# Kernel tuning notes

Hardware: AMD Instinct MI355X
Metric: run time of the kernel (lower is better)

## Reference

```python
import jax, jax.numpy as jnp
import numpy as np

N = 50000      # nodes
E = 800000     # edges (avg degree 16)
NFEAT = 256
NHID = 128
NCLASS = 40
NLAYERS_MID = 13  # gc2..gc14


def setup_inputs() -> dict:
    key = jax.random.key(0)
    ks = jax.random.split(key, 16)
    stdv_h = 1.0 / np.sqrt(NHID)     # GraphConvolution stdv = 1/sqrt(out_features)
    stdv_c = 1.0 / np.sqrt(NCLASS)
    u = lambda k, shape, s: jax.random.uniform(k, shape, jnp.float32, -s, s)
    return {
        "x": jax.random.normal(ks[0], (N, NFEAT), jnp.float32),
        "edge_src": jax.random.randint(ks[1], (E,), 0, N, jnp.int32),
        "edge_dst": jax.random.randint(ks[2], (E,), 0, N, jnp.int32),
        "edge_weight": jax.random.uniform(ks[3], (E,), jnp.float32),
        # skip-branch linear (self.weight / self.bias)
        "W0": u(ks[4], (NFEAT, NHID), stdv_h),
        "b0": u(ks[5], (NHID,), stdv_h),
        # gc1: nfeat -> nhid
        "W1": u(ks[6], (NFEAT, NHID), stdv_h),
        "b1": u(ks[7], (NHID,), stdv_h),
        # gc2..gc14: nhid -> nhid, stacked
        "Wmid": u(ks[8], (NLAYERS_MID, NHID, NHID), stdv_h),
        "bmid": u(ks[9], (NLAYERS_MID, NHID), stdv_h),
        # gc15: 14*nhid -> nclass
        "W15": u(ks[10], (14 * NHID, NCLASS), stdv_c),
        "b15": u(ks[11], (NCLASS,), stdv_c),
    }


def reference(x, edge_src, edge_dst, edge_weight, W0, b0, W1, b1, Wmid, bmid, W15, b15):
    n = x.shape[0]

    def gcn(h, W, b):
        # support = h @ W ; out = spmm(adj, support) + b  (adj as weighted edge list)
        support = h @ W
        msgs = support[edge_src] * edge_weight[:, None]           # [E, d]
        agg = jax.ops.segment_sum(msgs, edge_dst, num_segments=n)  # [N, d]
        return agg + b

    z = x @ W0 + b0
    x1 = jax.nn.relu(gcn(x, W1, b1)) + z

    def step(h, Wb):
        W, b = Wb
        hn = jax.nn.relu(gcn(h, W, b)) + h
        return hn, hn

    _, xs = jax.lax.scan(step, x1, (Wmid, bmid))   # xs: [13, N, NHID] = x2..x14
    all_x = jnp.concatenate([x1[None], xs], axis=0)  # [14, N, NHID] = x1..x14
    # concat order in torch code: (x14, x13, ..., x1)
    x_cat = jnp.swapaxes(all_x[::-1], 0, 1).reshape(n, 14 * NHID)
    # dropout is identity in eval mode
    x15 = gcn(x_cat, W15, b15)
    return jax.nn.log_softmax(x15, axis=1)
```

## Files before the change

kernel.cpp:

```cpp
#include <hip/hip_runtime.h>
#include <stdint.h>

#define NN 50000
#define EE 800000
#define DH 128
#define NC 40
#define KCAT (14*DH)
#define CAP 64

typedef __bf16 bf16x8 __attribute__((ext_vector_type(8)));
typedef float floatx4 __attribute__((ext_vector_type(4)));

#define GLOAD_LDS16(gp, lp)                                                          \
  __builtin_amdgcn_global_load_lds(                                                  \
      (const __attribute__((address_space(1))) uint32_t*)(gp),                       \
      (__attribute__((address_space(3))) uint32_t*)(lp), 16, 0, 0)

__device__ __forceinline__ float bf2f(unsigned short u) {
  union { uint32_t i; float f; } v; v.i = ((uint32_t)u) << 16; return v.f;
}
__device__ __forceinline__ unsigned short f2bf(float f) {
  union { float f; uint32_t i; } v; v.f = f;
  uint32_t x = v.i;
  uint32_t r = (x + 0x7fffu + ((x >> 16) & 1u)) >> 16;
  return (unsigned short)r;
}

__global__ void init_counts_detect(int* counts, const unsigned short* xw) {
  int i = blockIdx.x * blockDim.x + threadIdx.x;
  if (i < NN) counts[i] = 0;
  if (blockIdx.x == 0) {
    int t = threadIdx.x;
    int wild = 0;
    for (int k = t; k < 4096; k += 256) {
      unsigned e = (xw[k] >> 7) & 0xFF;
      if (e >= 0x90) wild++;
    }
    __shared__ int red[256];
    red[t] = wild;
    __syncthreads();
    for (int s = 128; s > 0; s >>= 1) {
      if (t < s) red[t] += red[t + s];
      __syncthreads();
    }
    if (t == 0) counts[NN] = red[0];
  }
}

__global__ void convert_f4(const void* in, unsigned short* outp, int n4, const int* flag) {
  bool isf32 = (*flag) > 32;
  for (int i = blockIdx.x * blockDim.x + threadIdx.x; i < n4;
       i += gridDim.x * blockDim.x) {
    ushort4 o;
    if (isf32) {
      float4 v = ((const float4*)in)[i];
      o.x = f2bf(v.x); o.y = f2bf(v.y); o.z = f2bf(v.z); o.w = f2bf(v.w);
    } else {
      o = ((const ushort4*)in)[i];
    }
    ((ushort4*)outp)[i] = o;
  }
}

__global__ void convert_bias(const void* b0, const void* b1, const void* bm,
                             const void* b15, unsigned short* bb, const int* flag) {
  bool isf32 = (*flag) > 32;
  int i = blockIdx.x * blockDim.x + threadIdx.x;
  if (i >= 1960) return;
  const void* src; int off;
  if (i < 128)        { src = b0;  off = i; }
  else if (i < 256)   { src = b1;  off = i - 128; }
  else if (i < 1920)  { src = bm;  off = i - 256; }
  else                { src = b15; off = i - 1920; }
  bb[i] = isf32 ? f2bf(((const float*)src)[off]) : ((const unsigned short*)src)[off];
}

__global__ void transpose_w(const void* B, unsigned short* BT,
                            int L, int K, int M, int Mpad, const int* flag) {
  bool isf32 = (*flag) > 32;
  int total = L * Mpad * K;
  for (int idx = blockIdx.x * blockDim.x + threadIdx.x; idx < total;
       idx += gridDim.x * blockDim.x) {
    int k = idx % K;
    int n = (idx / K) % Mpad;
    int l = idx / (K * Mpad);
    unsigned short v = 0;
    if (n < M) {
      size_t si = (size_t)l * K * M + (size_t)k * M + n;
      v = isf32 ? f2bf(((const float*)B)[si]) : ((const unsigned short*)B)[si];
    }
    BT[idx] = v;
  }
}

__global__ void build_ell(const int* __restrict__ src, const int* __restrict__ dst,
                          const void* __restrict__ w,
                          int* __restrict__ cnt, int2* __restrict__ ell,
                          const int* __restrict__ flag) {
  bool isf32 = (*flag) > 32;
  int e = blockIdx.x * blockDim.x + threadIdx.x;
  if (e >= EE) return;
  int d = dst[e];
  if ((unsigned)d >= NN) return;
  int p = atomicAdd(&cnt[d], 1);
  if (p >= CAP) return;
  int s = src[e];
  float wf = isf32 ? ((const float*)w)[e] : bf2f(((const unsigned short*)w)[e]);
  if ((unsigned)s >= NN) { s = 0; wf = 0.f; }
  union { float f; int i; } wv; wv.f = wf;
  ell[(size_t)d * CAP + p] = make_int2(s, wv.i);
}

__global__ __launch_bounds__(256) void gemm_first(
    const unsigned short* __restrict__ A,
    const unsigned short* __restrict__ BT,
    unsigned short* __restrict__ C0,
    unsigned short* __restrict__ C1,
    const unsigned short* __restrict__ bias) {
  __shared__ unsigned short As[64 * 256];
  int t = threadIdx.x;
  int wave = t >> 6, lane = t & 63;
  int q = lane >> 4, mn = lane & 15;
  int r0 = blockIdx.x * 64;

  #pragma unroll
  for (int cc = 0; cc < 8; ++cc) {
    int L = cc * 4096 + t * 16;
    int row = L >> 9;
    int colb = (L & 511) ^ ((row & 7) << 4);
    int gr = r0 + row; if (gr >= NN) gr = NN - 1;
    GLOAD_LDS16((const char*)A + (size_t)gr * 512 + colb, (char*)As + L);
  }
  __syncthreads();

  floatx4 acc[4][4];
  floatx4 zf = {0.f, 0.f, 0.f, 0.f};
  #pragma unroll
  for (int i = 0; i < 4; ++i)
    #pragma unroll
    for (int j = 0; j < 4; ++j) acc[i][j] = zf;

  #pragma unroll
  for (int ks = 0; ks < 8; ++ks) {
    bf16x8 fa[4], fb[4];
    #pragma unroll
    for (int i = 0; i < 4; ++i) {
      int row = i * 16 + mn;
      fa[i] = *(const bf16x8*)((const char*)As + row * 512 +
                               ((ks * 64 + q * 16) ^ ((row & 7) << 4)));
    }
    #pragma unroll
    for (int j = 0; j < 4; ++j)
      fb[j] = *(const bf16x8*)((const char*)BT +
                               (size_t)(wave * 64 + j * 16 + mn) * 512 + ks * 64 + q * 16);
    #pragma unroll
    for (int i = 0; i < 4; ++i)
      #pragma unroll
      for (int j = 0; j < 4; ++j)
        acc[i][j] = __builtin_amdgcn_mfma_f32_16x16x32_bf16(fa[i], fb[j], acc[i][j], 0, 0, 0);
  }

  #pragma unroll
  for (int j = 0; j < 4; ++j) {
    int col = wave * 64 + j * 16 + mn;
    bool is0 = col < 128;
    int ccol = is0 ? col : col - 128;
    unsigned short* Cp = is0 ? C0 : C1;
    float badd = is0 ? bf2f(bias[ccol]) : 0.f;
    #pragma unroll
    for (int i = 0; i < 4; ++i) {
      int rbase = r0 + i * 16 + q * 4;
      #pragma unroll
      for (int rr = 0; rr < 4; ++rr) {
        int row = rbase + rr;
        if (row < NN) Cp[(size_t)row * 128 + ccol] = f2bf(acc[i][j][rr] + badd);
      }
    }
  }
}

__global__ __launch_bounds__(256) void gemm_mid(
    const unsigned short* __restrict__ A,
    const unsigned short* __restrict__ BT,
    unsigned short* __restrict__ C) {
  __shared__ unsigned short As[32 * 128];
  int t = threadIdx.x;
  int wave = t >> 6, lane = t & 63;
  int q = lane >> 4, mn = lane & 15;
  int r0 = blockIdx.x * 32;

  #pragma unroll
  for (int cc = 0; cc < 2; ++cc) {
    int L = cc * 4096 + t * 16;
    int row = L >> 8;
    int colb = (L & 255) ^ ((row & 7) << 4);
    int gr = r0 + row; if (gr >= NN) gr = NN - 1;
    GLOAD_LDS16((const char*)A + (size_t)gr * (KCAT * 2) + colb, (char*)As + L);
  }
  __syncthreads();

  floatx4 acc[2][2];
  floatx4 zf = {0.f, 0.f, 0.f, 0.f};
  #pragma unroll
  for (int i = 0; i < 2; ++i)
    #pragma unroll
    for (int j = 0; j < 2; ++j) acc[i][j] = zf;

  #pragma unroll
  for (int ks = 0; ks < 4; ++ks) {
    bf16x8 fa[2], fb[2];
    #pragma unroll
    for (int i = 0; i < 2; ++i) {
      int row = i * 16 + mn;
      fa[i] = *(const bf16x8*)((const char*)As + row * 256 +
                               ((ks * 64 + q * 16) ^ ((row & 7) << 4)));
    }
    #pragma unroll
    for (int j = 0; j < 2; ++j)
      fb[j] = *(const bf16x8*)((const char*)BT +
                               (size_t)(wave * 32 + j * 16 + mn) * 256 + ks * 64 + q * 16);
    #pragma unroll
    for (int i = 0; i < 2; ++i)
      #pragma unroll
      for (int j = 0; j < 2; ++j)
        acc[i][j] = __builtin_amdgcn_mfma_f32_16x16x32_bf16(fa[i], fb[j], acc[i][j], 0, 0, 0);
  }

  #pragma unroll
  for (int i = 0; i < 2; ++i) {
    int rbase = r0 + i * 16 + q * 4;
    #pragma unroll
    for (int j = 0; j < 2; ++j) {
      int col = wave * 32 + j * 16 + mn;
      #pragma unroll
      for (int rr = 0; rr < 4; ++rr) {
        int row = rbase + rr;
        if (row < NN) C[(size_t)row * 128 + col] = f2bf(acc[i][j][rr]);
      }
    }
  }
}

__global__ __launch_bounds__(256) void gemm_cat2(
    const unsigned short* __restrict__ A,
    const unsigned short* __restrict__ BT,
    float* __restrict__ C) {
  __shared__ unsigned short As[2][64 * 128];
  int t = threadIdx.x;
  int wave = t >> 6, lane = t & 63;
  int q = lane >> 4, mn = lane & 15;
  int r0 = blockIdx.x * 64;

  floatx4 acc[3];
  floatx4 zf = {0.f, 0.f, 0.f, 0.f};
  #pragma unroll
  for (int j = 0; j < 3; ++j) acc[j] = zf;

  auto stage = [&](int c) {
    #pragma unroll
    for (int cc = 0; cc < 4; ++cc) {
      int L = cc * 4096 + t * 16;
      int row = L >> 8;
      int colb = (L & 255) ^ ((row & 7) << 4);
      int gr = r0 + row; if (gr >= NN) gr = NN - 1;
      GLOAD_LDS16((const char*)A + (size_t)gr * 3584 + c * 256 + colb,
                  (char*)As[c & 1] + L);
    }
  };

  stage(0);
  __syncthreads();
  for (int c = 0; c < 14; ++c) {
    if (c + 1 < 14) stage(c + 1);
    const char* buf = (const char*)As[c & 1];
    int rloc = wave * 16 + mn;
    int rsw = (rloc & 7) << 4;
    #pragma unroll
    for (int ks = 0; ks < 4; ++ks) {
      bf16x8 fa = *(const bf16x8*)(buf + rloc * 256 + ((ks * 64 + q * 16) ^ rsw));
      bf16x8 fb[3];
      #pragma unroll
      for (int j = 0; j < 3; ++j)
        fb[j] = *(const bf16x8*)((const char*)BT + (size_t)(j * 16 + mn) * 3584 +
                                 c * 256 + ks * 64 + q * 16);
      #pragma unroll
      for (int j = 0; j < 3; ++j)
        acc[j] = __builtin_amdgcn_mfma_f32_16x16x32_bf16(fa, fb[j], acc[j], 0, 0, 0);
    }
    if (c + 1 < 14) __syncthreads();
  }

  #pragma unroll
  for (int j = 0; j < 3; ++j) {
    int col = j * 16 + mn;
    if (col < NC) {
      #pragma unroll
      for (int rr = 0; rr < 4; ++rr) {
        int row = r0 + wave * 16 + q * 4 + rr;
        if (row < NN) C[(size_t)row * NC + col] = acc[j][rr];
      }
    }
  }
}

__global__ __launch_bounds__(256) void spmm_layer(
    const unsigned short* __restrict__ support, const int* __restrict__ cnt,
    const int2* __restrict__ ell, const unsigned short* __restrict__ bias,
    const unsigned short* __restrict__ res, int res_stride,
    unsigned short* __restrict__ out, int out_stride) {
  int wave = threadIdx.x >> 6, lane = threadIdx.x & 63;
  int row = blockIdx.x * 4 + wave;
  if (row >= NN) return;
  int n = cnt[row];
  if (n > CAP) n = CAP;
  int2 ev = ell[(size_t)row * CAP + lane];
  float a0 = 0.f, a1 = 0.f;
  int j = 0;
  for (; j + 16 <= n; j += 16) {
    uint32_t g[16];
    int sidx[16];
    #pragma unroll
    for (int u = 0; u < 16; ++u) sidx[u] = __shfl(ev.x, j + u);
    #pragma unroll
    for (int u = 0; u < 16; ++u)
      g[u] = *(const uint32_t*)(support + (size_t)sidx[u] * DH + 2 * lane);
    #pragma unroll
    for (int u = 0; u < 16; ++u) {
      union { int i; float f; } wv; wv.i = __shfl(ev.y, j + u);
      a0 += wv.f * bf2f((unsigned short)(g[u] & 0xffff));
      a1 += wv.f * bf2f((unsigned short)(g[u] >> 16));
    }
  }
  for (; j + 8 <= n; j += 8) {
    uint32_t g[8];
    int sidx[8];
    #pragma unroll
    for (int u = 0; u < 8; ++u) sidx[u] = __shfl(ev.x, j + u);
    #pragma unroll
    for (int u = 0; u < 8; ++u)
      g[u] = *(const uint32_t*)(support + (size_t)sidx[u] * DH + 2 * lane);
    #pragma unroll
    for (int u = 0; u < 8; ++u) {
      union { int i; float f; } wv; wv.i = __shfl(ev.y, j + u);
      a0 += wv.f * bf2f((unsigned short)(g[u] & 0xffff));
      a1 += wv.f * bf2f((unsigned short)(g[u] >> 16));
    }
  }
  for (; j < n; ++j) {
    int s = __shfl(ev.x, j);
    union { int i; float f; } wv; wv.i = __shfl(ev.y, j);
    uint32_t g = *(const uint32_t*)(support + (size_t)s * DH + 2 * lane);
    a0 += wv.f * bf2f((unsigned short)(g & 0xffff));
    a1 += wv.f * bf2f((unsigned short)(g >> 16));
  }
  uint32_t bw = *(const uint32_t*)(bias + 2 * lane);
  uint32_t rw = *(const uint32_t*)(res + (size_t)row * res_stride + 2 * lane);
  float v0 = fmaxf(a0 + bf2f((unsigned short)(bw & 0xffff)), 0.f) +
             bf2f((unsigned short)(rw & 0xffff));
  float v1 = fmaxf(a1 + bf2f((unsigned short)(bw >> 16)), 0.f) +
             bf2f((unsigned short)(rw >> 16));
  uint32_t o = (uint32_t)f2bf(v0) | ((uint32_t)f2bf(v1) << 16);
  *(uint32_t*)(out + (size_t)row * out_stride + 2 * lane) = o;
}

__global__ __launch_bounds__(256) void spmm_softmax_out(
    const float* __restrict__ s15, const int* __restrict__ cnt,
    const int2* __restrict__ ell, const unsigned short* __restrict__ bias,
    float* __restrict__ out) {
  int wave = threadIdx.x >> 6, lane = threadIdx.x & 63;
  int row = blockIdx.x * 4 + wave;
  if (row >= NN) return;
  int n = cnt[row];
  if (n > CAP) n = CAP;
  int2 ev = ell[(size_t)row * CAP + lane];
  int fl = lane < NC ? lane : NC - 1;
  float acc = 0.f;
  int j = 0;
  for (; j + 4 <= n; j += 4) {
    float g[4];
    #pragma unroll
    for (int u = 0; u < 4; ++u) {
      int s = __shfl(ev.x, j + u);
      g[u] = s15[(size_t)s * NC + fl];
    }
    #pragma unroll
    for (int u = 0; u < 4; ++u) {
      union { int i; float f; } wv; wv.i = __shfl(ev.y, j + u);
      acc += wv.f * g[u];
    }
  }
  for (; j < n; ++j) {
    int s = __shfl(ev.x, j);
    union { int i; float f; } wv; wv.i = __shfl(ev.y, j);
    acc += wv.f * s15[(size_t)s * NC + fl];
  }
  acc += bf2f(bias[fl]);
  float v = (lane < NC) ? acc : -3.0e38f;
  float m = v;
  #pragma unroll
  for (int off = 32; off > 0; off >>= 1) m = fmaxf(m, __shfl_xor(m, off));
  float e = (lane < NC) ? expf(v - m) : 0.f;
  float sum = e;
  #pragma unroll
  for (int off = 32; off > 0; off >>= 1) sum += __shfl_xor(sum, off);
  if (lane < NC) out[(size_t)row * NC + lane] = v - m - logf(sum);
}

extern "C" void kernel_launch(void* const* d_in, const int* in_sizes, int n_in,
                              void* d_out, int out_size, void* d_ws, size_t ws_size,
                              hipStream_t stream) {
  const void* x   = d_in[0];
  const int* esrc = (const int*)d_in[1];
  const int* edst = (const int*)d_in[2];
  const void* ew  = d_in[3];
  const void* W0  = d_in[4];
  const void* b0  = d_in[5];
  const void* W1  = d_in[6];
  const void* b1  = d_in[7];
  const void* Wm  = d_in[8];
  const void* bm  = d_in[9];
  const void* W15 = d_in[10];
  const void* b15 = d_in[11];
  float* out = (float*)d_out;

  char* ws = (char*)d_ws;
  size_t off = 0;
  auto alloc = [&](size_t bytes) -> void* {
    void* p = ws + off;
    off = (off + bytes + 255) & ~(size_t)255;
    return p;
  };
  unsigned short* xcat = (unsigned short*)alloc((size_t)NN * KCAT * 2);
  unsigned short* xbf  = (unsigned short*)alloc((size_t)NN * 256 * 2);
  unsigned short* supp = (unsigned short*)alloc((size_t)NN * DH * 2);
  unsigned short* zbuf = (unsigned short*)alloc((size_t)NN * DH * 2);
  float* s15           = (float*)alloc((size_t)NN * NC * 4);
  int* counts          = (int*)alloc((size_t)(NN + 1) * 4);
  int2* ell            = (int2*)alloc((size_t)NN * CAP * 8);
  unsigned short* W01T = (unsigned short*)alloc((size_t)256 * 256 * 2);
  unsigned short* WmT  = (unsigned short*)alloc((size_t)13 * 128 * 128 * 2);
  unsigned short* W15T = (unsigned short*)alloc((size_t)48 * 1792 * 2);
  unsigned short* bb   = (unsigned short*)alloc((size_t)(128 + 128 + 13 * 128 + 40) * 2);
  if (off > ws_size) return;
  int* flag = counts + NN;
  unsigned short* b0b  = bb;
  unsigned short* b1b  = bb + 128;
  unsigned short* bmb  = bb + 256;
  unsigned short* b15b = bb + 256 + 13 * 128;

  init_counts_detect<<<197, 256, 0, stream>>>(counts, (const unsigned short*)x);
  transpose_w<<<128, 256, 0, stream>>>(W0, W01T, 1, 256, 128, 128, flag);
  transpose_w<<<128, 256, 0, stream>>>(W1, W01T + 128 * 256, 1, 256, 128, 128, flag);
  transpose_w<<<832, 256, 0, stream>>>(Wm, WmT, 13, 128, 128, 128, flag);
  transpose_w<<<336, 256, 0, stream>>>(W15, W15T, 1, 1792, 40, 48, flag);
  convert_f4<<<2048, 256, 0, stream>>>(x, xbf, NN * 256 / 4, flag);
  convert_bias<<<8, 256, 0, stream>>>(b0, b1, bm, b15, bb, flag);
  build_ell<<<3125, 256, 0, stream>>>(esrc, edst, ew, counts, ell, flag);

  int gb64 = (NN + 63) / 64;
  int gb32 = (NN + 31) / 32;
  int sb   = (NN + 3) / 4;
  gemm_first<<<gb64, 256, 0, stream>>>(xbf, W01T, zbuf, supp, b0b);
  spmm_layer<<<sb, 256, 0, stream>>>(supp, counts, ell, b1b, zbuf, DH,
                                     xcat + 13 * DH, KCAT);
  for (int l = 0; l < 13; ++l) {
    gemm_mid<<<gb32, 256, 0, stream>>>(xcat + (13 - l) * DH,
                                       WmT + l * 128 * 128, supp);
    spmm_layer<<<sb, 256, 0, stream>>>(supp, counts, ell, bmb + l * DH,
                                       xcat + (13 - l) * DH, KCAT,
                                       xcat + (12 - l) * DH, KCAT);
  }
  gemm_cat2<<<gb64, 256, 0, stream>>>(xcat, W15T, s15);
  spmm_softmax_out<<<sb, 256, 0, stream>>>(s15, counts, ell, b15b, out);
}
```

Measured before the change: 1.017 ms.

## Pad ELL rows to multiples of eight and double-buffer SpMM gathers

Adds a pad_ell kernel that zero-fills each node's ELL slots up to the next multiple of eight. This lets the SpMM kernels drop their remainder loops and run only 8-wide batches. spmm_layer now ping-pongs two register batches so the next eight gathers are in flight while the current eight are accumulated, and it loads bias and residual early. The final concat GEMM preloads all B fragments for a chunk into registers before staging the next A tile. The cost is one extra launch, padded work on short rows (padded entries point at row 0 with zero weight), and higher register pressure.

After: 956.8 us. 1.06x faster.

```diff
diff --git a/kernel.cpp b/kernel.cpp
--- a/kernel.cpp
+++ b/kernel.cpp
@@ -111,6 +111,16 @@
   ell[(size_t)d * CAP + p] = make_int2(s, wv.i);
 }
 
+__global__ void pad_ell(const int* __restrict__ cnt, int2* __restrict__ ell) {
+  int wave = threadIdx.x >> 6, lane = threadIdx.x & 63;
+  int row = blockIdx.x * 4 + wave;
+  if (row >= NN) return;
+  int n = cnt[row];
+  if (n > CAP) n = CAP;
+  int padn = (n + 7) & ~7;
+  if (lane >= n && lane < padn) ell[(size_t)row * CAP + lane] = make_int2(0, 0);
+}
+
 __global__ __launch_bounds__(256) void gemm_first(
     const unsigned short* __restrict__ A,
     const unsigned short* __restrict__ BT,
@@ -241,7 +251,7 @@
   }
 }
 
-__global__ __launch_bounds__(256) void gemm_cat2(
+__global__ __launch_bounds__(256) void gemm_cat3(
     const unsigned short* __restrict__ A,
     const unsigned short* __restrict__ BT,
     float* __restrict__ C) {
@@ -256,6 +266,11 @@
   #pragma unroll
   for (int j = 0; j < 3; ++j) acc[j] = zf;
 
+  const char* bbase[3];
+  #pragma unroll
+  for (int j = 0; j < 3; ++j)
+    bbase[j] = (const char*)BT + (size_t)(j * 16 + mn) * 3584 + q * 16;
+
   auto stage = [&](int c) {
     #pragma unroll
     for (int cc = 0; cc < 4; ++cc) {
@@ -270,22 +285,25 @@
 
   stage(0);
   __syncthreads();
+  int rloc = wave * 16 + mn;
+  int rsw = (rloc & 7) << 4;
   for (int c = 0; c < 14; ++c) {
+    bf16x8 fb[3][4];
+    #pragma unroll
+    for (int ks = 0; ks < 4; ++ks)
+      #pragma unroll
+      for (int j = 0; j < 3; ++j)
+        fb[j][ks] = *(const bf16x8*)(bbase[j] + c * 256 + ks * 64);
+    asm volatile("" ::: "memory");
     if (c + 1 < 14) stage(c + 1);
+    asm volatile("" ::: "memory");
     const char* buf = (const char*)As[c & 1];
-    int rloc = wave * 16 + mn;
-    int rsw = (rloc & 7) << 4;
     #pragma unroll
     for (int ks = 0; ks < 4; ++ks) {
       bf16x8 fa = *(const bf16x8*)(buf + rloc * 256 + ((ks * 64 + q * 16) ^ rsw));
-      bf16x8 fb[3];
       #pragma unroll
       for (int j = 0; j < 3; ++j)
-        fb[j] = *(const bf16x8*)((const char*)BT + (size_t)(j * 16 + mn) * 3584 +
-                                 c * 256 + ks * 64 + q * 16);
-      #pragma unroll
-      for (int j = 0; j < 3; ++j)
-        acc[j] = __builtin_amdgcn_mfma_f32_16x16x32_bf16(fa, fb[j], acc[j], 0, 0, 0);
+        acc[j] = __builtin_amdgcn_mfma_f32_16x16x32_bf16(fa, fb[j][ks], acc[j], 0, 0, 0);
     }
     if (c + 1 < 14) __syncthreads();
   }
@@ -313,48 +331,42 @@
   if (row >= NN) return;
   int n = cnt[row];
   if (n > CAP) n = CAP;
-  int2 ev = ell[(size_t)row * CAP + lane];
+  int padn = (n + 7) & ~7;
+  int2 ev = make_int2(0, 0);
+  if (lane < padn) ev = ell[(size_t)row * CAP + lane];
+  uint32_t bw = *(const uint32_t*)(bias + 2 * lane);
+  uint32_t rw = *(const uint32_t*)(res + (size_t)row * res_stride + 2 * lane);
+
   float a0 = 0.f, a1 = 0.f;
-  int j = 0;
-  for (; j + 16 <= n; j += 16) {
-    uint32_t g[16];
-    int sidx[16];
-    #pragma unroll
-    for (int u = 0; u < 16; ++u) sidx[u] = __shfl(ev.x, j + u);
-    #pragma unroll
-    for (int u = 0; u < 16; ++u)
-      g[u] = *(const uint32_t*)(support + (size_t)sidx[u] * DH + 2 * lane);
-    #pragma unroll
-    for (int u = 0; u < 16; ++u) {
-      union { int i; float f; } wv; wv.i = __shfl(ev.y, j + u);
+  uint32_t gA[8], gB[8];
+  auto load8 = [&](uint32_t* g, int j0) {
+    #pragma unroll
+    for (int u = 0; u < 8; ++u) {
+      int s = __shfl(ev.x, j0 + u);
+      g[u] = *(const uint32_t*)(support + (size_t)s * DH + 2 * lane);
+    }
+  };
+  auto fma8 = [&](const uint32_t* g, int j0) {
+    #pragma unroll
+    for (int u = 0; u < 8; ++u) {
+      union { int i; float f; } wv; wv.i = __shfl(ev.y, j0 + u);
       a0 += wv.f * bf2f((unsigned short)(g[u] & 0xffff));
       a1 += wv.f * bf2f((unsigned short)(g[u] >> 16));
     }
-  }
-  for (; j + 8 <= n; j += 8) {
-    uint32_t g[8];
-    int sidx[8];
-    #pragma unroll
-    for (int u = 0; u < 8; ++u) sidx[u] = __shfl(ev.x, j + u);
-    #pragma unroll
-    for (int u = 0; u < 8; ++u)
-      g[u] = *(const uint32_t*)(support + (size_t)sidx[u] * DH + 2 * lane);
-    #pragma unroll
-    for (int u = 0; u < 8; ++u) {
-      union { int i; float f; } wv; wv.i = __shfl(ev.y, j + u);
-      a0 += wv.f * bf2f((unsigned short)(g[u] & 0xffff));
-      a1 += wv.f * bf2f((unsigned short)(g[u] >> 16));
-    }
-  }
-  for (; j < n; ++j) {
-    int s = __shfl(ev.x, j);
-    union { int i; float f; } wv; wv.i = __shfl(ev.y, j);
-    uint32_t g = *(const uint32_t*)(support + (size_t)s * DH + 2 * lane);
-    a0 += wv.f * bf2f((unsigned short)(g & 0xffff));
-    a1 += wv.f * bf2f((unsigned short)(g >> 16));
-  }
-  uint32_t bw = *(const uint32_t*)(bias + 2 * lane);
-  uint32_t rw = *(const uint32_t*)(res + (size_t)row * res_stride + 2 * lane);
+  };
+  if (padn > 0) {
+    load8(gA, 0);
+    int b = 0;
+    for (;;) {
+      if (8 * (b + 1) < padn) load8(gB, 8 * (b + 1));
+      fma8(gA, 8 * b);
+      ++b; if (8 * b >= padn) break;
+      if (8 * (b + 1) < padn) load8(gA, 8 * (b + 1));
+      fma8(gB, 8 * b);
+      ++b; if (8 * b >= padn) break;
+    }
+  }
+
   float v0 = fmaxf(a0 + bf2f((unsigned short)(bw & 0xffff)), 0.f) +
              bf2f((unsigned short)(rw & 0xffff));
   float v1 = fmaxf(a1 + bf2f((unsigned short)(bw >> 16)), 0.f) +
@@ -372,11 +384,12 @@
   if (row >= NN) return;
   int n = cnt[row];
   if (n > CAP) n = CAP;
-  int2 ev = ell[(size_t)row * CAP + lane];
+  int padn = (n + 7) & ~7;
+  int2 ev = make_int2(0, 0);
+  if (lane < padn) ev = ell[(size_t)row * CAP + lane];
   int fl = lane < NC ? lane : NC - 1;
   float acc = 0.f;
-  int j = 0;
-  for (; j + 4 <= n; j += 4) {
+  for (int j = 0; j < padn; j += 4) {
     float g[4];
     #pragma unroll
     for (int u = 0; u < 4; ++u) {
@@ -388,11 +401,6 @@
       union { int i; float f; } wv; wv.i = __shfl(ev.y, j + u);
       acc += wv.f * g[u];
     }
-  }
-  for (; j < n; ++j) {
-    int s = __shfl(ev.x, j);
-    union { int i; float f; } wv; wv.i = __shfl(ev.y, j);
-    acc += wv.f * s15[(size_t)s * NC + fl];
   }
   acc += bf2f(bias[fl]);
   float v = (lane < NC) ? acc : -3.0e38f;
@@ -460,6 +468,7 @@
   int gb64 = (NN + 63) / 64;
   int gb32 = (NN + 31) / 32;
   int sb   = (NN + 3) / 4;
+  pad_ell<<<sb, 256, 0, stream>>>(counts, ell);
   gemm_first<<<gb64, 256, 0, stream>>>(xbf, W01T, zbuf, supp, b0b);
   spmm_layer<<<sb, 256, 0, stream>>>(supp, counts, ell, b1b, zbuf, DH,
                                      xcat + 13 * DH, KCAT);
@@ -470,6 +479,6 @@
                                        xcat + (13 - l) * DH, KCAT,
                                        xcat + (12 - l) * DH, KCAT);
   }
-  gemm_cat2<<<gb64, 256, 0, stream>>>(xcat, W15T, s15);
+  gemm_cat3<<<gb64, 256, 0, stream>>>(xcat, W15T, s15);
   spmm_softmax_out<<<sb, 256, 0, stream>>>(s15, counts, ell, b15b, out);
 }
```
